# Kernel tuning notes

Hardware: AMD Instinct MI355X
Metric: run time of the kernel (lower is better)

The kernel has to match this reference:

```python
import jax, jax.numpy as jnp
import numpy as np

D_MODEL = 1024
N_HEADS = 16
HEAD_DIM = D_MODEL // N_HEADS
WINDOW = 256


def setup_inputs() -> dict:
    key = jax.random.key(0)
    ks = jax.random.split(key, 5)
    s = 1.0 / np.sqrt(D_MODEL)
    x = jax.random.normal(ks[0], (1, 4096, D_MODEL), dtype=jnp.float32)
    W_qkv = jax.random.uniform(ks[1], (D_MODEL, 3 * D_MODEL), jnp.float32, -s, s)
    b_qkv = jax.random.uniform(ks[2], (3 * D_MODEL,), jnp.float32, -s, s)
    W_proj = jax.random.uniform(ks[3], (D_MODEL, D_MODEL), jnp.float32, -s, s)
    b_proj = jax.random.uniform(ks[4], (D_MODEL,), jnp.float32, -s, s)
    return {"x": x, "W_qkv": W_qkv, "b_qkv": b_qkv, "W_proj": W_proj, "b_proj": b_proj}


def reference(x, W_qkv, b_qkv, W_proj, b_proj):
    b, t, c = x.shape
    qkv = x @ W_qkv + b_qkv  # [b,t,3c]
    q, k, v = jnp.split(qkv, 3, axis=-1)
    # [b,h,t,d]
    q = q.reshape(b, t, N_HEADS, HEAD_DIM).transpose(0, 2, 1, 3)
    k = k.reshape(b, t, N_HEADS, HEAD_DIM).transpose(0, 2, 1, 3)
    v = v.reshape(b, t, N_HEADS, HEAD_DIM).transpose(0, 2, 1, 3)
    att = jnp.einsum('bhqd,bhkd->bhqk', q, k) / np.sqrt(HEAD_DIM)
    idx = jnp.arange(t)
    diff = idx[:, None] - idx[None, :]  # query - key
    allowed = (diff >= 0) & (diff < WINDOW)  # causal & local window
    att = jnp.where(allowed[None, None], att, -jnp.inf)
    att = jax.nn.softmax(att, axis=-1)
    y = jnp.einsum('bhqk,bhkd->bhqd', att, v)
    y = y.transpose(0, 2, 1, 3).reshape(b, t, c)
    return y @ W_proj + b_proj
```

## Files before the change

### kernel.cpp

```cpp
#include <hip/hip_runtime.h>
#include <stdint.h>

#define TSEQ 4096
#define DMODEL 1024
#define N3 3072
#define NHEADS 16
#define HDIM 64
#define WINDOW 256

typedef __attribute__((ext_vector_type(8))) short short8;
typedef __attribute__((ext_vector_type(4))) float f32x4;

__device__ __forceinline__ unsigned short f2bf(float f) {
  unsigned u = __builtin_bit_cast(unsigned, f);
  return (unsigned short)((u + 0x7fffu + ((u >> 16) & 1u)) >> 16);
}

__device__ __forceinline__ unsigned cvtpk(float lo, float hi) {
  unsigned r;
  asm("v_cvt_pk_bf16_f32 %0, %1, %2" : "=v"(r) : "v"(lo), "v"(hi));
  return r;
}

__device__ __forceinline__ f32x4 mfma16(short8 a, short8 b, f32x4 c) {
  return __builtin_amdgcn_mfma_f32_16x16x32_bf16(a, b, c, 0, 0, 0);
}

__device__ __forceinline__ void g2lds16(const void* g, void* l) {
  __builtin_amdgcn_global_load_lds(
      (const __attribute__((address_space(1))) void*)(uintptr_t)g,
      (__attribute__((address_space(3))) void*)(uintptr_t)l,
      16, 0, 0);
}


__global__ __launch_bounds__(256) void cvt_f32_bf16_v4(const float* __restrict__ in,
                                                       unsigned short* __restrict__ out) {
  int i = (blockIdx.x * 256 + threadIdx.x) * 4;
  float4 v = *(const float4*)(in + i);
  unsigned lo = cvtpk(v.x, v.y), hi = cvtpk(v.z, v.w);
  unsigned long long packed = (unsigned long long)lo | ((unsigned long long)hi << 32);
  *(unsigned long long*)(out + i) = packed;
}

__global__ __launch_bounds__(256) void transpose_cvt2(const float* __restrict__ Wqkv,
                                                      const float* __restrict__ Wproj,
                                                      unsigned short* __restrict__ oQkvT,
                                                      unsigned short* __restrict__ oProjT) {
  __shared__ float tile[32][33];
  int bx = blockIdx.x;
  const float* in;
  unsigned short* out;
  int C;
  if (bx < 96) {
    in = Wqkv; out = oQkvT; C = N3;
  } else {
    bx -= 96; in = Wproj; out = oProjT; C = DMODEL;
  }
  const int R = DMODEL;
  int c0 = bx * 32;
  int r0 = blockIdx.y * 32;
  int tx = threadIdx.x, ty = threadIdx.y;
#pragma unroll
  for (int i = 0; i < 32; i += 8)
    tile[ty + i][tx] = in[(size_t)(r0 + ty + i) * C + c0 + tx];
  __syncthreads();
#pragma unroll
  for (int i = 0; i < 32; i += 8)
    out[(size_t)(c0 + ty + i) * R + r0 + tx] = f2bf(tile[tx][ty + i]);
}


template <int EPI>
__global__ __launch_bounds__(256)
void gemm_bf16_128(const unsigned short* __restrict__ A,
                   const unsigned short* __restrict__ BT,
                   const float* __restrict__ bias,
                   unsigned short* __restrict__ oQ,
                   unsigned short* __restrict__ oK,
                   unsigned short* __restrict__ oVT,
                   float* __restrict__ oF) {
  __shared__ unsigned short Asm[2][128 * 32];
  __shared__ unsigned short Bsm[2][128 * 32];
  const int K = 1024;
  int m0 = blockIdx.x * 128;
  int n0 = blockIdx.y * 128;
  int tid = threadIdx.x;
  int w = tid >> 6, lane = tid & 63;
  int l15 = lane & 15, l4 = lane >> 4;
  int wm = (w >> 1) * 64, wn = (w & 1) * 64;

  f32x4 acc[4][4];
#pragma unroll
  for (int i = 0; i < 4; i++)
#pragma unroll
    for (int j = 0; j < 4; j++) acc[i][j] = (f32x4){0.f, 0.f, 0.f, 0.f};

  const unsigned short* aSrc = A + (size_t)(m0 + w * 32 + (lane >> 2)) * K + (lane & 3) * 8;
  const unsigned short* bSrc = BT + (size_t)(n0 + w * 32 + (lane >> 2)) * K + (lane & 3) * 8;

  for (int k0 = 0; k0 < K; k0 += 64) {
#pragma unroll
    for (int hf = 0; hf < 2; hf++) {
      g2lds16(aSrc + k0 + hf * 32, &Asm[hf][(w * 2 + 0) * 512]);
      g2lds16(aSrc + 16 * K + k0 + hf * 32, &Asm[hf][(w * 2 + 1) * 512]);
      g2lds16(bSrc + k0 + hf * 32, &Bsm[hf][(w * 2 + 0) * 512]);
      g2lds16(bSrc + 16 * K + k0 + hf * 32, &Bsm[hf][(w * 2 + 1) * 512]);
    }
    __syncthreads();
#pragma unroll
    for (int hf = 0; hf < 2; hf++) {
      short8 af[4], bfr[4];
#pragma unroll
      for (int mi = 0; mi < 4; mi++)
        af[mi] = *(const short8*)&Asm[hf][(wm + mi * 16 + l15) * 32 + l4 * 8];
#pragma unroll
      for (int ni = 0; ni < 4; ni++)
        bfr[ni] = *(const short8*)&Bsm[hf][(wn + ni * 16 + l15) * 32 + l4 * 8];
#pragma unroll
      for (int mi = 0; mi < 4; mi++)
#pragma unroll
        for (int ni = 0; ni < 4; ni++)
          acc[mi][ni] = mfma16(af[mi], bfr[ni], acc[mi][ni]);
    }
    __syncthreads();
  }

#pragma unroll
  for (int ni = 0; ni < 4; ni++) {
    int nn = n0 + wn + ni * 16 + l15;
    float bv = bias[nn];
    int c = nn & 1023;
    int hh = c >> 6, dd = c & 63;
#pragma unroll
    for (int mi = 0; mi < 4; mi++) {
      int mm = m0 + wm + mi * 16 + l4 * 4;
      float v0 = acc[mi][ni][0] + bv;
      float v1 = acc[mi][ni][1] + bv;
      float v2 = acc[mi][ni][2] + bv;
      float v3 = acc[mi][ni][3] + bv;
      if (EPI == 1) {
        oF[(size_t)(mm + 0) * 1024 + nn] = v0;
        oF[(size_t)(mm + 1) * 1024 + nn] = v1;
        oF[(size_t)(mm + 2) * 1024 + nn] = v2;
        oF[(size_t)(mm + 3) * 1024 + nn] = v3;
      } else if (nn < 1024) {
        oQ[((size_t)hh * TSEQ + mm + 0) * 64 + dd] = f2bf(v0 * 0.125f);
        oQ[((size_t)hh * TSEQ + mm + 1) * 64 + dd] = f2bf(v1 * 0.125f);
        oQ[((size_t)hh * TSEQ + mm + 2) * 64 + dd] = f2bf(v2 * 0.125f);
        oQ[((size_t)hh * TSEQ + mm + 3) * 64 + dd] = f2bf(v3 * 0.125f);
      } else if (nn < 2048) {
        oK[((size_t)hh * TSEQ + mm + 0) * 64 + dd] = f2bf(v0);
        oK[((size_t)hh * TSEQ + mm + 1) * 64 + dd] = f2bf(v1);
        oK[((size_t)hh * TSEQ + mm + 2) * 64 + dd] = f2bf(v2);
        oK[((size_t)hh * TSEQ + mm + 3) * 64 + dd] = f2bf(v3);
      } else {
        unsigned lo = cvtpk(v0, v1), hi = cvtpk(v2, v3);
        unsigned long long pv = (unsigned long long)lo | ((unsigned long long)hi << 32);
        *(unsigned long long*)(oVT + ((size_t)hh * 64 + dd) * TSEQ + mm) = pv;
      }
    }
  }
}


__global__ __launch_bounds__(256)
void attn_swa(const unsigned short* __restrict__ Qa,
              const unsigned short* __restrict__ Ka,
              const unsigned short* __restrict__ Vt,
              unsigned short* __restrict__ Y) {
  __shared__ __align__(16) char KV[2][16384];
  __shared__ __align__(16) unsigned char Pl[4][2048];
  int flat = blockIdx.x;
  int swz = (flat & 7) * 128 + (flat >> 3);
  int h = swz >> 6, qb = swz & 63;
  int w = threadIdx.x >> 6, lane = threadIdx.x & 63;
  int l15 = lane & 15, l4 = lane >> 4;
  int qrow0 = qb * 64 + w * 16;
  int q = qrow0 + l15;

  const unsigned short* qp = Qa + ((size_t)h * TSEQ + q) * 64 + l4 * 8;
  short8 qf0 = *(const short8*)qp;
  short8 qf1 = *(const short8*)(qp + 32);

  const char* kgb = (const char*)(Ka + (size_t)h * TSEQ * 64);
  const char* vgb = (const char*)(Vt + (size_t)h * 64 * TSEQ);

  auto stage = [&](int kt, int b) {
    int kbase = kt * 64;
    int sub = lane >> 3, slot = (lane & 7) * 16;
    if (w < 2) {
      int R0 = w * 32;
      const char* src = kgb + (size_t)kbase * 128;
#pragma unroll
      for (int j = 0; j < 4; j++) {
        int r = R0 + j * 8 + sub;
        g2lds16(src + r * 128 + (slot ^ ((r & 7) << 4)), &KV[b][R0 * 128 + j * 1024]);
      }
    } else {
      int D0 = (w - 2) * 32;
      const char* src = vgb + (size_t)kbase * 2;
#pragma unroll
      for (int j = 0; j < 4; j++) {
        int d = D0 + j * 8 + sub;
        g2lds16(src + (size_t)d * 8192 + (slot ^ ((d & 7) << 4)),
                &KV[b][8192 + D0 * 128 + j * 1024]);
      }
    }
  };

  float m = -1e30f, lsum = 0.f;
  f32x4 o[4];
#pragma unroll
  for (int ni = 0; ni < 4; ni++) o[ni] = (f32x4){0.f, 0.f, 0.f, 0.f};

  unsigned char* pw = Pl[w];
  int xw = (l15 & 7) << 4;

  auto compute = [&](int kt, int b, int MODE) {
    int kbase = kt * 64;
    const char* kb = KV[b];
    const char* vb = KV[b] + 8192;
    f32x4 s[4];
#pragma unroll
    for (int ni = 0; ni < 4; ni++) {
      int rb = (ni * 16 + l15) * 128;
      short8 k0 = *(const short8*)(kb + rb + ((l4 * 16) ^ xw));
      short8 k1 = *(const short8*)(kb + rb + ((64 + l4 * 16) ^ xw));
      f32x4 z = (f32x4){0.f, 0.f, 0.f, 0.f};
      z = mfma16(k0, qf0, z);
      s[ni] = mfma16(k1, qf1, z);
    }
    if (MODE != 0) {
#pragma unroll
      for (int ni = 0; ni < 4; ni++)
#pragma unroll
        for (int r = 0; r < 4; r++) {
          int key = kbase + ni * 16 + l4 * 4 + r;
          bool ok = (MODE == 2) ? (key <= q) : (q - key < WINDOW);
          s[ni][r] = ok ? s[ni][r] : -1e30f;
        }
    }
    float pm0 = fmaxf(fmaxf(s[0][0], s[0][1]), fmaxf(s[0][2], s[0][3]));
    float pm1 = fmaxf(fmaxf(s[1][0], s[1][1]), fmaxf(s[1][2], s[1][3]));
    float pm2 = fmaxf(fmaxf(s[2][0], s[2][1]), fmaxf(s[2][2], s[2][3]));
    float pm3 = fmaxf(fmaxf(s[3][0], s[3][1]), fmaxf(s[3][2], s[3][3]));
    float pm = fmaxf(fmaxf(pm0, pm1), fmaxf(pm2, pm3));
    pm = fmaxf(pm, __shfl_xor(pm, 16, 64));
    pm = fmaxf(pm, __shfl_xor(pm, 32, 64));
    float mn = fmaxf(m, pm);
    float alpha = __expf(m - mn);
    m = mn;
    float rs = 0.f;
#pragma unroll
    for (int ni = 0; ni < 4; ni++)
#pragma unroll
      for (int r = 0; r < 4; r++) {
        float p = __expf(s[ni][r] - mn);
        s[ni][r] = p;
        rs += p;
      }
    rs += __shfl_xor(rs, 16, 64);
    rs += __shfl_xor(rs, 32, 64);
    lsum = lsum * alpha + rs;
#pragma unroll
    for (int ni = 0; ni < 4; ni++) {
      unsigned lo = cvtpk(s[ni][0], s[ni][1]);
      unsigned hi = cvtpk(s[ni][2], s[ni][3]);
      unsigned long long pv = (unsigned long long)lo | ((unsigned long long)hi << 32);
      *(unsigned long long*)(pw + l15 * 128 + ((ni * 32 + l4 * 8) ^ xw)) = pv;
    }
    short8 pa0 = *(const short8*)(pw + l15 * 128 + ((l4 * 16) ^ xw));
    short8 pa1 = *(const short8*)(pw + l15 * 128 + ((64 + l4 * 16) ^ xw));
#pragma unroll
    for (int ni = 0; ni < 4; ni++)
#pragma unroll
      for (int r = 0; r < 4; r++) o[ni][r] *= alpha;
#pragma unroll
    for (int ni = 0; ni < 4; ni++) {
      int rb = (ni * 16 + l15) * 128;
      short8 v0 = *(const short8*)(vb + rb + ((l4 * 16) ^ xw));
      short8 v1 = *(const short8*)(vb + rb + ((64 + l4 * 16) ^ xw));
      o[ni] = mfma16(v0, pa0, o[ni]);
      o[ni] = mfma16(v1, pa1, o[ni]);
    }
  };

  int kt0 = qb >= 4 ? qb - 4 : 0;
  int NT = qb - kt0 + 1;
  stage(kt0, 0);
  for (int t = 0; t < NT; t++) {
    int kt = kt0 + t;
    if (t + 1 < NT) {
      stage(kt + 1, (t + 1) & 1);
      asm volatile("s_waitcnt vmcnt(4)" ::: "memory");
    } else {
      asm volatile("s_waitcnt vmcnt(0)" ::: "memory");
    }
    __builtin_amdgcn_s_barrier();
    __builtin_amdgcn_sched_barrier(0);
    int MODE = (t == NT - 1) ? 2 : ((qb >= 4 && t == 0) ? 1 : 0);
    compute(kt, t & 1, MODE);
    __builtin_amdgcn_sched_barrier(0);
    __builtin_amdgcn_s_barrier();
  }

  float inv = 1.f / lsum;
#pragma unroll
  for (int ni = 0; ni < 4; ni++) {
    unsigned lo = cvtpk(o[ni][0] * inv, o[ni][1] * inv);
    unsigned hi = cvtpk(o[ni][2] * inv, o[ni][3] * inv);
    unsigned long long yv = (unsigned long long)lo | ((unsigned long long)hi << 32);
    *(unsigned long long*)(Y + (size_t)q * DMODEL + h * 64 + ni * 16 + l4 * 4) = yv;
  }
}


extern "C" void kernel_launch(void* const* d_in, const int* in_sizes, int n_in,
                              void* d_out, int out_size, void* d_ws, size_t ws_size,
                              hipStream_t stream) {
  const float* x = (const float*)d_in[0];
  const float* Wqkv = (const float*)d_in[1];
  const float* bqkv = (const float*)d_in[2];
  const float* Wproj = (const float*)d_in[3];
  const float* bproj = (const float*)d_in[4];
  float* out = (float*)d_out;

  unsigned short* ws = (unsigned short*)d_ws;
  unsigned short* xb = ws;
  unsigned short* wqkvT = xb + (size_t)TSEQ * DMODEL;
  unsigned short* wprojT = wqkvT + (size_t)N3 * DMODEL;
  unsigned short* qarr = wprojT + (size_t)DMODEL * DMODEL;
  unsigned short* karr = qarr + (size_t)NHEADS * TSEQ * HDIM;
  unsigned short* vtarr = karr + (size_t)NHEADS * TSEQ * HDIM;
  unsigned short* yarr = vtarr + (size_t)NHEADS * TSEQ * HDIM;

  cvt_f32_bf16_v4<<<(TSEQ * DMODEL) / 1024, 256, 0, stream>>>(x, xb);
  transpose_cvt2<<<dim3(128, 32), dim3(32, 8), 0, stream>>>(Wqkv, Wproj, wqkvT, wprojT);
  gemm_bf16_128<0><<<dim3(TSEQ / 128, N3 / 128), 256, 0, stream>>>(xb, wqkvT, bqkv, qarr, karr, vtarr, nullptr);
  attn_swa<<<1024, 256, 0, stream>>>(qarr, karr, vtarr, yarr);
  gemm_bf16_128<1><<<dim3(TSEQ / 128, DMODEL / 128), 256, 0, stream>>>(yarr, wprojT, bproj, nullptr, nullptr, nullptr, out);
}
```

Before: 96.56 us.

## Double-buffer GEMM K-loop with prefetch and XOR-swizzled LDS layout

Restructures the GEMM main loop so the next 32-wide K slice is prefetched into the alternate LDS buffer while the current one is computed, using explicit vmcnt waits and raw barriers instead of load-then-sync per 64-wide step. It also applies an XOR swizzle to LDS slot placement on both the load and fragment-read sides to reduce bank conflicts. The intent is to hide global-to-LDS latency and cut LDS conflicts. In exchange there are twice as many barrier pairs per K, and correctness depends on the vmcnt accounting matching the number of outstanding loads.

After: 85.55 us. -11.4%, faster.

```diff
diff --git a/kernel.cpp b/kernel.cpp
--- a/kernel.cpp
+++ b/kernel.cpp
@@ -96,34 +96,55 @@
 #pragma unroll
     for (int j = 0; j < 4; j++) acc[i][j] = (f32x4){0.f, 0.f, 0.f, 0.f};
 
-  const unsigned short* aSrc = A + (size_t)(m0 + w * 32 + (lane >> 2)) * K + (lane & 3) * 8;
-  const unsigned short* bSrc = BT + (size_t)(n0 + w * 32 + (lane >> 2)) * K + (lane & 3) * 8;
-
-  for (int k0 = 0; k0 < K; k0 += 64) {
-#pragma unroll
-    for (int hf = 0; hf < 2; hf++) {
-      g2lds16(aSrc + k0 + hf * 32, &Asm[hf][(w * 2 + 0) * 512]);
-      g2lds16(aSrc + 16 * K + k0 + hf * 32, &Asm[hf][(w * 2 + 1) * 512]);
-      g2lds16(bSrc + k0 + hf * 32, &Bsm[hf][(w * 2 + 0) * 512]);
-      g2lds16(bSrc + 16 * K + k0 + hf * 32, &Bsm[hf][(w * 2 + 1) * 512]);
-    }
-    __syncthreads();
-#pragma unroll
-    for (int hf = 0; hf < 2; hf++) {
-      short8 af[4], bfr[4];
-#pragma unroll
-      for (int mi = 0; mi < 4; mi++)
-        af[mi] = *(const short8*)&Asm[hf][(wm + mi * 16 + l15) * 32 + l4 * 8];
+  int lr = lane >> 2;
+  int slot = ((lane & 3) * 16) ^ (((lr >> 1) & 3) << 4);
+  const char* aG = (const char*)(A + (size_t)(m0 + w * 32 + lr) * K) + slot;
+  const char* bG = (const char*)(BT + (size_t)(n0 + w * 32 + lr) * K) + slot;
+  const size_t rowSkip = (size_t)16 * K * 2;
+
+  auto stage = [&](int s, int b) {
+    int koff = s * 64;
+    g2lds16(aG + koff, &Asm[b][w * 1024]);
+    g2lds16(aG + rowSkip + koff, &Asm[b][w * 1024 + 512]);
+    g2lds16(bG + koff, &Bsm[b][w * 1024]);
+    g2lds16(bG + rowSkip + koff, &Bsm[b][w * 1024 + 512]);
+  };
+
+  int sX = ((l15 >> 1) & 3) << 4;
+
+  auto compute = [&](int b) {
+    short8 af[4], bfr[4];
+#pragma unroll
+    for (int mi = 0; mi < 4; mi++) {
+      int rA = wm + mi * 16 + l15;
+      af[mi] = *(const short8*)((const char*)Asm[b] + rA * 64 + ((l4 * 16) ^ sX));
+    }
+#pragma unroll
+    for (int ni = 0; ni < 4; ni++) {
+      int rB = wn + ni * 16 + l15;
+      bfr[ni] = *(const short8*)((const char*)Bsm[b] + rB * 64 + ((l4 * 16) ^ sX));
+    }
+#pragma unroll
+    for (int mi = 0; mi < 4; mi++)
 #pragma unroll
       for (int ni = 0; ni < 4; ni++)
-        bfr[ni] = *(const short8*)&Bsm[hf][(wn + ni * 16 + l15) * 32 + l4 * 8];
-#pragma unroll
-      for (int mi = 0; mi < 4; mi++)
-#pragma unroll
-        for (int ni = 0; ni < 4; ni++)
-          acc[mi][ni] = mfma16(af[mi], bfr[ni], acc[mi][ni]);
-    }
-    __syncthreads();
+        acc[mi][ni] = mfma16(af[mi], bfr[ni], acc[mi][ni]);
+  };
+
+  const int NS = K / 32;
+  stage(0, 0);
+  for (int s = 0; s < NS; s++) {
+    if (s + 1 < NS) {
+      stage(s + 1, (s + 1) & 1);
+      asm volatile("s_waitcnt vmcnt(4)" ::: "memory");
+    } else {
+      asm volatile("s_waitcnt vmcnt(0)" ::: "memory");
+    }
+    __builtin_amdgcn_s_barrier();
+    __builtin_amdgcn_sched_barrier(0);
+    compute(s & 1);
+    __builtin_amdgcn_sched_barrier(0);
+    __builtin_amdgcn_s_barrier();
   }
 
 #pragma unroll
```
